# Kernel optimization log

Measured on AMD Instinct MI355X. Metric: run time of the kernel, lower is better.

Reference implementation:

```python
import jax, jax.numpy as jnp
import numpy as np

H, F, K, R = 8, 64, 10, 256  # num_heads, in_features, num_sines, num_realizations
B, L = 4, 2048


def setup_inputs() -> dict:
    key = jax.random.key(0)
    k1, k2, k3, k4, k5, k6 = jax.random.split(key, 6)
    return {
        "queries": jax.random.normal(k1, (B, L, H, F), dtype=jnp.float32),
        "keys": jax.random.normal(k2, (B, L, H, F), dtype=jnp.float32),
        "z": jax.random.normal(k3, (B, H, F, 2 * K, R), dtype=jnp.float32),
        "freqs": jax.random.normal(k4, (H, F, K), dtype=jnp.float32),
        "offsets": jax.random.normal(k5, (H, F, K), dtype=jnp.float32),
        "gains": jax.random.normal(k6, (H, F, K), dtype=jnp.float32),
    }


def reference(queries, keys, z, freqs, offsets, gains):
    h, f_dim, k_sines = freqs.shape
    length = queries.shape[1]
    r = z.shape[-1]
    # split positional / non-positional features (rest is empty here: key_dim == in_features)
    q_pos, q_rest = queries[..., :f_dim], queries[..., f_dim:]
    k_pos, k_rest = keys[..., :f_dim], keys[..., f_dim:]

    idx = jnp.arange(length, dtype=queries.dtype)  # linspace(0, L-1, L)
    fr = jax.nn.sigmoid(freqs)[:, :, None, :] / 2.0          # [H, F, 1, K]
    base = 2.0 * jnp.pi * fr * idx[None, None, :, None]       # [H, F, L, K]
    ph_q = base + offsets[:, :, None, :]
    ph_k = base
    # stack(cos, sin) on last axis then flatten -> interleaved cos0,sin0,... : [H, F, L, 2K]
    omega_q = jnp.stack([jnp.cos(ph_q), jnp.sin(ph_q)], axis=-1).reshape(h, f_dim, length, 2 * k_sines)
    omega_k = jnp.stack([jnp.cos(ph_k), jnp.sin(ph_k)], axis=-1).reshape(h, f_dim, length, 2 * k_sines)

    g = jnp.tile(jax.nn.softplus(gains), (1, 1, 2))           # [H, F, 2K] (block-repeated, as in torch .repeat)
    zs = z * g[None, :, :, :, None] / np.sqrt(r * f_dim).astype(np.float32)  # [B, H, F, 2K, R]

    # fused double contraction over f (in_features) and s (2K sines); equals
    # (omega @ z) permuted then multiplied by queries and summed over in_features
    qhat = jnp.einsum('hfls,bhfsr,blhf->blhr', omega_q, zs, q_pos)  # [B, L, H, R]
    khat = jnp.einsum('hfls,bhfsr,blhf->blhr', omega_k, zs, k_pos)

    qhat = jnp.concatenate([qhat, q_rest], axis=-1)
    khat = jnp.concatenate([khat, k_rest], axis=-1)
    return qhat, khat
```

## Files before the change

kernel.cpp:

```cpp
#include <hip/hip_runtime.h>
#include <math.h>


#define NH 8
#define NF 64
#define NK 10
#define NR 256
#define NB 4
#define NL 2048
#define KTOT 1280
#define BM 128
#define BK 32
#define NCH (KTOT/BK)
#define NFRAG_B 16
#define WS_NEEDED ((size_t)NB*NH*NCH*NFRAG_B*1024)

typedef __attribute__((ext_vector_type(8))) short short8;
typedef __attribute__((ext_vector_type(4))) float f32x4;
typedef __attribute__((ext_vector_type(4))) unsigned int u32x4;
typedef __attribute__((ext_vector_type(2))) unsigned int u32x2;

static __device__ __forceinline__ unsigned short f2b(float f) {
    unsigned x = __float_as_uint(f);
    return (unsigned short)((x + 0x7FFFu + ((x >> 16) & 1u)) >> 16);
}
static __device__ __forceinline__ unsigned int pk2(float a, float b) {
    return (unsigned int)f2b(a) | ((unsigned int)f2b(b) << 16);
}
static __device__ __forceinline__ unsigned int cvtpk(float lo, float hi) {
    unsigned int r;
    asm("v_cvt_pk_bf16_f32 %0, %1, %2" : "=v"(r) : "v"(lo), "v"(hi));
    return r;
}
static __device__ __forceinline__ void gload_lds16(const void* g, void* l) {
    __builtin_amdgcn_global_load_lds(
        (const __attribute__((address_space(1))) unsigned int*)g,
        (__attribute__((address_space(3))) unsigned int*)l, 16, 0, 0);
}

__global__ __launch_bounds__(256)
void spe_prep(const float* __restrict__ z, const float* __restrict__ gains,
              unsigned char* __restrict__ bpack)
{
    __shared__ float s_g[NF*NK];
    const int ch  = blockIdx.x;
    const int bh  = blockIdx.y;
    const int h   = bh & 7;
    const int tid = threadIdx.x;
    for (int i = tid; i < NF*NK; i += 256)
        s_g[i] = log1pf(expf(gains[h*NF*NK + i])) * 0.0078125f;
    __syncthreads();
    const float* zb = z + (size_t)bh * KTOT * NR;
    unsigned char* dst = bpack + ((size_t)(bh*NCH + ch) * NFRAG_B) * 1024;
    #pragma unroll
    for (int it = 0; it < 4; ++it) {
        const int s  = tid + 256*it;
        const int fi = s >> 6;
        const int l  = s & 63;
        const int r  = fi*16 + (l & 15);
        const int k0 = ch*BK + (l >> 4)*8;
        u32x4 wv;
        #pragma unroll
        for (int jp = 0; jp < 4; ++jp) {
            const int ka = k0 + 2*jp, kb = ka + 1;
            const int fa = (ka*3277) >> 16; int sa = ka - fa*20; if (sa >= NK) sa -= NK;
            const int fb = (kb*3277) >> 16; int sb = kb - fb*20; if (sb >= NK) sb -= NK;
            const float va = zb[(size_t)ka*NR + r] * s_g[fa*NK + sa];
            const float vb = zb[(size_t)kb*NR + r] * s_g[fb*NK + sb];
            wv[jp] = pk2(va, vb);
        }
        *(u32x4*)(dst + (size_t)s*16) = wv;
    }
}

#define OFF_B0  0
#define OFF_B1  16384
#define OFF_A   32768
#define OFF_POS 49152
#define OFF_FR  65536
#define OFF_CO  68096
#define OFF_SO  70656
#define SMEM_SZ 73216

__global__ __launch_bounds__(512, 4)
void spe_main(const float* __restrict__ queries, const float* __restrict__ keys,
              const float* __restrict__ freqs, const float* __restrict__ offsets,
              const unsigned char* __restrict__ bpack, float* __restrict__ out)
{
    __shared__ __attribute__((aligned(16))) unsigned char smem[SMEM_SZ];
    const int tid  = threadIdx.x;
    const int lane = tid & 63;
    const int w    = tid >> 6;

    const int fb = blockIdx.x;
    const int h  = fb & 7;
    const int b  = (fb >> 3) & 3;
    const int l0 = (fb >> 5) * 64;
    const int bh = b*NH + h;

    float* ld_fr = (float*)(smem + OFF_FR);
    float* ld_co = (float*)(smem + OFF_CO);
    float* ld_so = (float*)(smem + OFF_SO);
    unsigned short* pos_t = (unsigned short*)(smem + OFF_POS);

    for (int i = tid; i < NF*NK; i += 512) {
        const float fv = freqs[h*NF*NK + i];
        ld_fr[i] = 0.5f / (1.0f + expf(-fv));
        const float xo = __builtin_amdgcn_fractf(offsets[h*NF*NK + i] * 0.15915494309189535f);
        ld_co[i] = __builtin_amdgcn_cosf(xo);
        ld_so[i] = __builtin_amdgcn_sinf(xo);
    }
    {
        const int r  = tid >> 2;
        const int f0 = (tid & 3) * 16;
        const int rl = r & 63;
        const float* src = (r < 64)
            ? queries + ((size_t)((b*NL + l0 + rl)*NH + h))*NF + f0
            : keys    + ((size_t)((b*NL + l0 + rl)*NH + h))*NF + f0;
        unsigned short* pdst = pos_t + ((r >> 6) << 12);
        #pragma unroll
        for (int j = 0; j < 4; ++j) {
            const float4 v = *(const float4*)(src + j*4);
            const int f = f0 + j*4;
            pdst[(f+0)*64 + rl] = f2b(v.x);
            pdst[(f+1)*64 + rl] = f2b(v.y);
            pdst[(f+2)*64 + rl] = f2b(v.z);
            pdst[(f+3)*64 + rl] = f2b(v.w);
        }
    }
    __syncthreads();

    const unsigned char* bp = bpack + (size_t)bh * ((size_t)NCH*NFRAG_B*1024);

    const int fn0 = w * 2;

    auto issueB = [&](int t) {
        unsigned char* Bd = smem + ((t & 1) ? OFF_B1 : OFF_B0);
        const unsigned char* bsrc = bp + (size_t)t*NFRAG_B*1024;
        #pragma unroll
        for (int j = 0; j < 2; ++j)
            gload_lds16(bsrc + (size_t)(fn0 + j)*1024 + lane*16,
                        Bd + ((fn0 + j) << 10));
    };

    f32x4 acc[8][2];
    #pragma unroll
    for (int mi = 0; mi < 8; ++mi)
        #pragma unroll
        for (int ni = 0; ni < 2; ++ni)
            acc[mi][ni] = (f32x4){0.f, 0.f, 0.f, 0.f};

    const int rq   = tid & 63;
    const int oct  = (tid >> 6) & 3;
    const int half = tid >> 8;
    const float lf = (float)(l0 + rq);
    const unsigned short* posq = pos_t;
    const unsigned short* posk = pos_t + 4096;
    const int a_log_q = ((rq >> 4) << 10) + ((oct*16 + (rq & 15)) << 4) + (half << 3);
    const int aw_q = a_log_q ^ (((rq >> 4) & 3) << 5);
    const int aw_k = (a_log_q + 4096) ^ (((rq >> 4) & 3) << 5);

    auto synthA = [&](int t, u32x2& q01, u32x2& k01) {
        #pragma unroll
        for (int p = 0; p < 2; ++p) {
            const int kk   = t*BK + oct*8 + (half*2 + p)*2;
            const int f    = (kk*3277) >> 16;
            const int srem = kk - f*20;
            const int kidx = f*NK + (srem >> 1);
            const float x  = __builtin_amdgcn_fractf(ld_fr[kidx] * lf);
            const float ck = __builtin_amdgcn_cosf(x);
            const float sk = __builtin_amdgcn_sinf(x);
            const float co = ld_co[kidx], so = ld_so[kidx];
            const float cq = ck*co - sk*so;
            const float sq = sk*co + ck*so;
            const float pq = __uint_as_float(((unsigned)posq[f*64 + rq]) << 16);
            const float pk = __uint_as_float(((unsigned)posk[f*64 + rq]) << 16);
            q01[p] = cvtpk(cq*pq, sq*pq);
            k01[p] = cvtpk(ck*pk, sk*pk);
        }
    };

    u32x2 q01, k01;
    synthA(0, q01, k01);
    *(u32x2*)(smem + OFF_A + aw_q) = q01;
    *(u32x2*)(smem + OFF_A + aw_k) = k01;
    issueB(0);
    synthA(1, q01, k01);
    __builtin_amdgcn_sched_barrier(0);
    __builtin_amdgcn_s_barrier();
    __builtin_amdgcn_sched_barrier(0);

    #pragma unroll 1
    for (int t = 0; t < NCH; ++t) {
        const int par = t & 1;

        if (t + 1 < NCH) {
            const int np = (t + 1) & 1;
            *(u32x2*)(smem + OFF_A + np*8192 + aw_q) = q01;
            *(u32x2*)(smem + OFF_A + np*8192 + aw_k) = k01;
            issueB(t + 1);
        }
        if (t + 2 < NCH) synthA(t + 2, q01, k01);

        if (t + 1 < NCH) { asm volatile("s_waitcnt vmcnt(2)" ::: "memory"); }
        else             { asm volatile("s_waitcnt vmcnt(0)" ::: "memory"); }
        __builtin_amdgcn_sched_barrier(0);

        const unsigned char* Bc = smem + (par ? OFF_B1 : OFF_B0);
        short8 bf[2];
        #pragma unroll
        for (int ni = 0; ni < 2; ++ni)
            bf[ni] = *(const short8*)(Bc + ((fn0 + ni) << 10) + (lane << 4));

        __builtin_amdgcn_s_setprio(1);
        #pragma unroll
        for (int mi = 0; mi < 8; ++mi) {
            const int aoff = (mi << 10) + (lane << 4);
            const short8 af = *(const short8*)(smem + OFF_A + par*8192
                                               + (aoff ^ ((mi & 3) << 5)));
            #pragma unroll
            for (int ni = 0; ni < 2; ++ni)
                acc[mi][ni] = __builtin_amdgcn_mfma_f32_16x16x32_bf16(af, bf[ni], acc[mi][ni], 0, 0, 0);
        }
        __builtin_amdgcn_s_setprio(0);

        if (t + 1 < NCH) {
            __builtin_amdgcn_sched_barrier(0);
            __builtin_amdgcn_s_barrier();
            __builtin_amdgcn_sched_barrier(0);
        }
    }

    const size_t kofs = (size_t)NB*NL*NH*NR;
    const int row_l = (lane >> 4) * 4;
    const int col_r = lane & 15;
    #pragma unroll
    for (int mi = 0; mi < 8; ++mi) {
        const size_t qk_off = (mi >= 4) ? kofs : 0;
        const int lg = l0 + (mi & 3)*16 + row_l;
        #pragma unroll
        for (int ni = 0; ni < 2; ++ni) {
            const int rg = w*32 + ni*16 + col_r;
            const f32x4 v = acc[mi][ni];
            #pragma unroll
            for (int q = 0; q < 4; ++q)
                out[qk_off + ((size_t)((b*NL + lg + q)*NH + h))*NR + rg] = v[q];
        }
    }
}

#define FOFF_B   0
#define FOFF_A   32768
#define FOFF_POS 49152
#define FOFF_FR  65536
#define FOFF_OFS 68096
#define FOFF_GS  70656
#define FSMEM_SZ 73216

__global__ __launch_bounds__(512, 4)
void spe_mfma_fb(const float* __restrict__ queries, const float* __restrict__ keys,
                 const float* __restrict__ z, const float* __restrict__ freqs,
                 const float* __restrict__ offsets, const float* __restrict__ gains,
                 float* __restrict__ out)
{
    __shared__ __attribute__((aligned(16))) unsigned char smem[FSMEM_SZ];
    const int tid = threadIdx.x, lane = tid & 63;
    const int l0 = blockIdx.x * BM, bh = blockIdx.y;
    const int b = bh >> 3, h = bh & 7, isK = blockIdx.z;
    float* ld_fr = (float*)(smem + FOFF_FR);
    float* ld_of = (float*)(smem + FOFF_OFS);
    float* ld_gs = (float*)(smem + FOFF_GS);
    unsigned short* pos_t = (unsigned short*)(smem + FOFF_POS);
    for (int i = tid; i < NF*NK; i += 512) {
        const float fv = freqs[h*NF*NK + i];
        ld_fr[i] = 0.5f / (1.0f + expf(-fv));
        ld_of[i] = isK ? 0.0f : offsets[h*NF*NK + i] * 0.15915494309189535f;
        ld_gs[i] = log1pf(expf(gains[h*NF*NK + i])) * 0.0078125f;
    }
    {
        const float* pos = isK ? keys : queries;
        #pragma unroll
        for (int i = 0; i < 4; ++i) {
            const int lrow = (tid >> 4) + 32*i;
            const int f0 = (tid & 15) * 4;
            const float4 v = *(const float4*)(pos + ((size_t)((b*NL + l0 + lrow)*NH + h))*NF + f0);
            pos_t[(f0+0)*BM + lrow] = f2b(v.x); pos_t[(f0+1)*BM + lrow] = f2b(v.y);
            pos_t[(f0+2)*BM + lrow] = f2b(v.z); pos_t[(f0+3)*BM + lrow] = f2b(v.w);
        }
    }
    __syncthreads();
    const int w = tid >> 6, wm = w >> 2, wn = w & 3;
    f32x4 acc[4][4];
    #pragma unroll
    for (int mi = 0; mi < 4; ++mi)
        #pragma unroll
        for (int ni = 0; ni < 4; ++ni) acc[mi][ni] = (f32x4){0.f,0.f,0.f,0.f};
    const float* zbh = z + (size_t)(b*NH + h) * ((size_t)KTOT*NR);
    for (int ch = 0; ch < KTOT/64; ++ch) {
        const int fs0 = ch * 64;
        #pragma unroll
        for (int i = 0; i < 4; ++i) {
            const int tau = tid + 512*i, r = tau & 255, krun = tau >> 8;
            const float* zp = zbh + (size_t)(fs0 + krun*8)*NR + r;
            u32x4 wv2;
            #pragma unroll
            for (int jp = 0; jp < 4; ++jp) {
                const int fs = fs0 + krun*8 + 2*jp;
                const int f = (fs*3277) >> 16; const int rem = fs - f*20;
                const int km = (rem >= NK) ? rem - NK : rem;
                const int kn = ((rem+1) >= NK && (rem+1) < 2*NK) ? rem+1-NK : rem+1;
                const float sc0 = ld_gs[f*NK + km], sc1 = ld_gs[f*NK + (kn < NK ? kn : kn-NK)];
                wv2[jp] = pk2(zp[(2*jp)*NR]*sc0, zp[(2*jp+1)*NR]*sc1);
            }
            *(u32x4*)(smem + FOFF_B + ((((krun>>2)*16) + (r>>4)) << 10)
                                    + ((((krun&3)*16) + (r&15)) << 4)) = wv2;
        }
        #pragma unroll
        for (int i = 0; i < 2; ++i) {
            const int tau = tid + 512*i, m = tau & 127, krun = tau >> 7;
            const float lff = (float)(l0 + m);
            u32x4 wv2;
            #pragma unroll
            for (int jp = 0; jp < 4; ++jp) {
                const int fs = fs0 + krun*8 + 2*jp;
                const int f = (fs*3277) >> 16; const int rem = fs - f*20;
                const int kidx = f*NK + (rem >> 1);
                const float x = __builtin_amdgcn_fractf(ld_of[kidx] + ld_fr[kidx]*lff);
                const float c = __builtin_amdgcn_cosf(x), sn = __builtin_amdgcn_sinf(x);
                const float p = __uint_as_float(((unsigned)pos_t[f*BM + m]) << 16);
                wv2[jp] = pk2(c*p, sn*p);
            }
            *(u32x4*)(smem + FOFF_A + ((((krun>>2)*8) + (m>>4)) << 10)
                                    + ((((krun&3)*16) + (m&15)) << 4)) = wv2;
        }
        __syncthreads();
        #pragma unroll
        for (int ks = 0; ks < 2; ++ks) {
            short8 bf[4];
            #pragma unroll
            for (int ni = 0; ni < 4; ++ni)
                bf[ni] = *(const short8*)(smem + FOFF_B + ((ks*16 + wn*4 + ni) << 10) + (lane << 4));
            #pragma unroll
            for (int mi = 0; mi < 4; ++mi) {
                const short8 af = *(const short8*)(smem + FOFF_A + ((ks*8 + wm*4 + mi) << 10) + (lane << 4));
                #pragma unroll
                for (int ni = 0; ni < 4; ++ni)
                    acc[mi][ni] = __builtin_amdgcn_mfma_f32_16x16x32_bf16(af, bf[ni], acc[mi][ni], 0, 0, 0);
            }
        }
        __syncthreads();
    }
    const size_t qk_off = (size_t)isK * ((size_t)NB*NL*NH*NR);
    const int row_l = (lane >> 4) * 4, col_r = lane & 15;
    #pragma unroll
    for (int mi = 0; mi < 4; ++mi) {
        const int lg = l0 + wm*64 + mi*16 + row_l;
        #pragma unroll
        for (int ni = 0; ni < 4; ++ni) {
            const int rg = wn*64 + ni*16 + col_r;
            const f32x4 v = acc[mi][ni];
            #pragma unroll
            for (int q = 0; q < 4; ++q)
                out[qk_off + ((size_t)((b*NL + lg + q)*NH + h))*NR + rg] = v[q];
        }
    }
}

extern "C" void kernel_launch(void* const* d_in, const int* in_sizes, int n_in,
                              void* d_out, int out_size, void* d_ws, size_t ws_size,
                              hipStream_t stream) {
    const float* queries = (const float*)d_in[0];
    const float* keys    = (const float*)d_in[1];
    const float* z       = (const float*)d_in[2];
    const float* freqs   = (const float*)d_in[3];
    const float* offsets = (const float*)d_in[4];
    const float* gains   = (const float*)d_in[5];
    float* out = (float*)d_out;

    if (ws_size >= WS_NEEDED) {
        unsigned char* bpack = (unsigned char*)d_ws;
        spe_prep<<<dim3(NCH, NB*NH), 256, 0, stream>>>(z, gains, bpack);
        spe_main<<<dim3(1024), 512, 0, stream>>>(queries, keys, freqs, offsets, bpack, out);
    } else {
        spe_mfma_fb<<<dim3(NL/BM, NB*NH, 2), 512, 0, stream>>>(queries, keys, z, freqs, offsets, gains, out);
    }
}
```

Measured before the change: 123.8 us.

## Precompute cos/sin tables in a separate kernel and stream them into main loop

Adds a kernel that precomputes per-head, per-position cos/sin of the key phases as packed bf16 into workspace, removing the per-chunk transcendental evaluation from the main MFMA kernel. The main kernel now prefetches these table entries from global memory two chunks ahead, overlapping them with the B-tile loads, and adjusts the wait count. This trades ALU work in the main loop for extra global traffic and an extra launch. It also rounds the key-phase cos/sin to bf16 before the query rotation is applied, which adds some precision loss.

```diff
diff --git a/kernel.cpp b/kernel.cpp
--- a/kernel.cpp
+++ b/kernel.cpp
@@ -13,7 +13,9 @@
 #define BK 32
 #define NCH (KTOT/BK)
 #define NFRAG_B 16
-#define WS_NEEDED ((size_t)NB*NH*NCH*NFRAG_B*1024)
+#define WS_BPACK ((size_t)NB*NH*NCH*NFRAG_B*1024)
+#define WS_TRIG  ((size_t)NH*NCH*8*2048*2*4)
+#define WS_NEED2 (WS_BPACK + WS_TRIG)
 
 typedef __attribute__((ext_vector_type(8))) short short8;
 typedef __attribute__((ext_vector_type(4))) float f32x4;
@@ -73,19 +75,51 @@
     }
 }
 
+__global__ __launch_bounds__(256)
+void spe_trig2(const float* __restrict__ freqs, unsigned int* __restrict__ trig)
+{
+    __shared__ float s_fr[16];
+    const int t = blockIdx.x;
+    const int h = blockIdx.y;
+    const int tid = threadIdx.x;
+    if (tid < 16) {
+        const float fv = freqs[h*640 + t*16 + tid];
+        s_fr[tid] = 0.5f / (1.0f + expf(-fv));
+    }
+    __syncthreads();
+    unsigned int* dst = trig + (size_t)(h*NCH + t) * (8*2048*2);
+    #pragma unroll 8
+    for (int it = 0; it < 64; ++it) {
+        const int site = tid + 256*it;
+        const int l    = site & 2047;
+        const int g    = site >> 11;
+        const int oct  = g & 3;
+        const int half = g >> 2;
+        const int kb   = oct*4 + half*2;
+        u32x2 wv;
+        #pragma unroll
+        for (int j = 0; j < 2; ++j) {
+            const float x = __builtin_amdgcn_fractf(s_fr[kb + j] * (float)l);
+            wv[j] = pk2(__builtin_amdgcn_cosf(x), __builtin_amdgcn_sinf(x));
+        }
+        *(u32x2*)(dst + ((size_t)g*2048 + l)*2) = wv;
+    }
+}
+
 #define OFF_B0  0
 #define OFF_B1  16384
 #define OFF_A   32768
 #define OFF_POS 49152
-#define OFF_FR  65536
 #define OFF_CO  68096
 #define OFF_SO  70656
 #define SMEM_SZ 73216
 
 __global__ __launch_bounds__(512, 4)
 void spe_main(const float* __restrict__ queries, const float* __restrict__ keys,
-              const float* __restrict__ freqs, const float* __restrict__ offsets,
-              const unsigned char* __restrict__ bpack, float* __restrict__ out)
+              const float* __restrict__ offsets,
+              const unsigned char* __restrict__ bpack,
+              const unsigned int* __restrict__ trig,
+              float* __restrict__ out)
 {
     __shared__ __attribute__((aligned(16))) unsigned char smem[SMEM_SZ];
     const int tid  = threadIdx.x;
@@ -98,14 +132,11 @@
     const int l0 = (fb >> 5) * 64;
     const int bh = b*NH + h;
 
-    float* ld_fr = (float*)(smem + OFF_FR);
     float* ld_co = (float*)(smem + OFF_CO);
     float* ld_so = (float*)(smem + OFF_SO);
     unsigned short* pos_t = (unsigned short*)(smem + OFF_POS);
 
     for (int i = tid; i < NF*NK; i += 512) {
-        const float fv = freqs[h*NF*NK + i];
-        ld_fr[i] = 0.5f / (1.0f + expf(-fv));
         const float xo = __builtin_amdgcn_fractf(offsets[h*NF*NK + i] * 0.15915494309189535f);
         ld_co[i] = __builtin_amdgcn_cosf(xo);
         ld_so[i] = __builtin_amdgcn_sinf(xo);
@@ -133,7 +164,6 @@
     const unsigned char* bp = bpack + (size_t)bh * ((size_t)NCH*NFRAG_B*1024);
 
     const int fn0 = w * 2;
-
     auto issueB = [&](int t) {
         unsigned char* Bd = smem + ((t & 1) ? OFF_B1 : OFF_B0);
         const unsigned char* bsrc = bp + (size_t)t*NFRAG_B*1024;
@@ -153,39 +183,46 @@
     const int rq   = tid & 63;
     const int oct  = (tid >> 6) & 3;
     const int half = tid >> 8;
-    const float lf = (float)(l0 + rq);
     const unsigned short* posq = pos_t;
     const unsigned short* posk = pos_t + 4096;
     const int a_log_q = ((rq >> 4) << 10) + ((oct*16 + (rq & 15)) << 4) + (half << 3);
     const int aw_q = a_log_q ^ (((rq >> 4) & 3) << 5);
     const int aw_k = (a_log_q + 4096) ^ (((rq >> 4) & 3) << 5);
 
-    auto synthA = [&](int t, u32x2& q01, u32x2& k01) {
+    const unsigned int* tbase = trig + (size_t)h * ((size_t)NCH*8*2048*2)
+                              + ((size_t)((half*4 + oct)*2048 + (l0 + rq)))*2;
+    const size_t tstep = (size_t)8*2048*2;
+
+    auto synthA = [&](int t, const u32x2 tr, u32x2& q01o, u32x2& k01o) {
         #pragma unroll
         for (int p = 0; p < 2; ++p) {
-            const int kk   = t*BK + oct*8 + (half*2 + p)*2;
-            const int f    = (kk*3277) >> 16;
-            const int srem = kk - f*20;
-            const int kidx = f*NK + (srem >> 1);
-            const float x  = __builtin_amdgcn_fractf(ld_fr[kidx] * lf);
-            const float ck = __builtin_amdgcn_cosf(x);
-            const float sk = __builtin_amdgcn_sinf(x);
+            const int kidx = t*16 + oct*4 + half*2 + p;
+            const int f    = (kidx * 6554) >> 16;
+            const float ck = __uint_as_float(tr[p] << 16);
+            const float sk = __uint_as_float(tr[p] & 0xffff0000u);
             const float co = ld_co[kidx], so = ld_so[kidx];
             const float cq = ck*co - sk*so;
             const float sq = sk*co + ck*so;
             const float pq = __uint_as_float(((unsigned)posq[f*64 + rq]) << 16);
             const float pk = __uint_as_float(((unsigned)posk[f*64 + rq]) << 16);
-            q01[p] = cvtpk(cq*pq, sq*pq);
-            k01[p] = cvtpk(ck*pk, sk*pk);
+            q01o[p] = cvtpk(cq*pq, sq*pq);
+            k01o[p] = cvtpk(ck*pk, sk*pk);
         }
     };
 
     u32x2 q01, k01;
-    synthA(0, q01, k01);
+    {
+        const u32x2 tr0 = *(const u32x2*)(tbase);
+        synthA(0, tr0, q01, k01);
+    }
     *(u32x2*)(smem + OFF_A + aw_q) = q01;
     *(u32x2*)(smem + OFF_A + aw_k) = k01;
     issueB(0);
-    synthA(1, q01, k01);
+    {
+        const u32x2 tr1 = *(const u32x2*)(tbase + tstep);
+        synthA(1, tr1, q01, k01);
+    }
+    u32x2 trCur = *(const u32x2*)(tbase + 2*tstep);
     __builtin_amdgcn_sched_barrier(0);
     __builtin_amdgcn_s_barrier();
     __builtin_amdgcn_sched_barrier(0);
@@ -200,9 +237,16 @@
             *(u32x2*)(smem + OFF_A + np*8192 + aw_k) = k01;
             issueB(t + 1);
         }
-        if (t + 2 < NCH) synthA(t + 2, q01, k01);
-
-        if (t + 1 < NCH) { asm volatile("s_waitcnt vmcnt(2)" ::: "memory"); }
+        __builtin_amdgcn_sched_barrier(0);
+
+        u32x2 trNew;
+        if (t + 1 < NCH) {
+            const int t3 = (t + 3 < NCH) ? t + 3 : NCH - 1;
+            trNew = *(const u32x2*)(tbase + (size_t)t3*tstep);
+        }
+        if (t + 2 < NCH) synthA(t + 2, trCur, q01, k01);
+
+        if (t + 1 < NCH) { asm volatile("s_waitcnt vmcnt(3)" ::: "memory"); }
         else             { asm volatile("s_waitcnt vmcnt(0)" ::: "memory"); }
         __builtin_amdgcn_sched_barrier(0);
 
@@ -228,6 +272,7 @@
             __builtin_amdgcn_sched_barrier(0);
             __builtin_amdgcn_s_barrier();
             __builtin_amdgcn_sched_barrier(0);
+            trCur = trNew;
         }
     }
 
@@ -377,10 +422,12 @@
     const float* gains   = (const float*)d_in[5];
     float* out = (float*)d_out;
 
-    if (ws_size >= WS_NEEDED) {
+    if (ws_size >= WS_NEED2) {
         unsigned char* bpack = (unsigned char*)d_ws;
+        unsigned int*  trig  = (unsigned int*)(bpack + WS_BPACK);
         spe_prep<<<dim3(NCH, NB*NH), 256, 0, stream>>>(z, gains, bpack);
-        spe_main<<<dim3(1024), 512, 0, stream>>>(queries, keys, freqs, offsets, bpack, out);
+        spe_trig2<<<dim3(NCH, NH), 256, 0, stream>>>(freqs, trig);
+        spe_main<<<dim3(1024), 512, 0, stream>>>(queries, keys, offsets, bpack, trig, out);
     } else {
         spe_mfma_fb<<<dim3(NL/BM, NB*NH, 2), 512, 0, stream>>>(queries, keys, z, freqs, offsets, gains, out);
     }
```

Measured after the change: 143.0 us. +15.5%, slower.
